# Performance work log

Measured on AMD Instinct MI355X. Metric: run time of the kernel, lower is better.

Reference implementation:

```python
import math
import jax, jax.numpy as jnp
import numpy as np

B, T, D_MODEL, HEAD_DIM = 4, 2048, 768, 64

def setup_inputs() -> dict:
    key = jax.random.key(0)
    ks = jax.random.split(key, 4)
    scale = 1.0 / math.sqrt(D_MODEL)
    return {
        "x": jax.random.normal(ks[0], (B, T, D_MODEL), dtype=jnp.float32),
        "Wq": jax.random.normal(ks[1], (D_MODEL, HEAD_DIM), dtype=jnp.float32) * scale,
        "bq": jnp.zeros((HEAD_DIM,), dtype=jnp.float32),
        "Wk": jax.random.normal(ks[2], (D_MODEL, HEAD_DIM), dtype=jnp.float32) * scale,
        "bk": jnp.zeros((HEAD_DIM,), dtype=jnp.float32),
        "Wv": jax.random.normal(ks[3], (D_MODEL, HEAD_DIM), dtype=jnp.float32) * scale,
        "bv": jnp.zeros((HEAD_DIM,), dtype=jnp.float32),
    }

def reference(x, Wq, bq, Wk, bk, Wv, bv):
    # Single causal self-attention head (dropout=0 / eval mode).
    q = x @ Wq + bq                      # [B, T, H]
    k = x @ Wk + bk                      # [B, T, H]
    v = x @ Wv + bv                      # [B, T, H]
    head_dim = q.shape[-1]
    scores = jnp.einsum("bth,bsh->bts", q, k) / math.sqrt(head_dim)  # [B, T, T]
    seq_len = x.shape[1]
    causal = jnp.tril(jnp.ones((seq_len, seq_len), dtype=bool))      # [T, T]
    scores = jnp.where(causal, scores, -jnp.inf)
    attn = jax.nn.softmax(scores, axis=-1)                           # [B, T, T]
    out = jnp.einsum("bts,bsh->bth", attn, v)                        # [B, T, H]
    return out
```

## Files before the change

### kernel.cpp

```cpp
#include <hip/hip_runtime.h>
#include <math.h>

#define BB 4
#define TT 2048
#define DM 768
#define HD 64
#define NROW (BB*TT)
#define WFRAG_HALF ((size_t)24*12*512)

typedef __attribute__((ext_vector_type(8))) short bf16x8;
typedef __attribute__((ext_vector_type(4))) float f32x4;

__device__ __forceinline__ unsigned short f2bf(float f) {
    unsigned int u = __float_as_uint(f);
    u += 0x7FFFu + ((u >> 16) & 1u);
    return (unsigned short)(u >> 16);
}
__device__ __forceinline__ float bf2f(unsigned short h) {
    return __uint_as_float(((unsigned int)h) << 16);
}

__global__ __launch_bounds__(256) void wconv_kernel(
    const float* __restrict__ Wq, const float* __restrict__ Wk,
    const float* __restrict__ Wv, unsigned short* __restrict__ wfrag)
{
    __shared__ float ws[32][69];
    const int blk = blockIdx.x;
    const int m = blk / 24, kc = blk % 24;
    const float* Wm = (m == 0) ? Wq : ((m == 1) ? Wk : Wv);
    const float sc = (m == 0) ? 0.125f : 1.0f;
    const int tid = threadIdx.x;
    {
        int r = tid >> 3, c0 = (tid & 7) * 8;
        *(float4*)&ws[r][c0]     = *(const float4*)(Wm + (size_t)(32*kc + r)*HD + c0);
        *(float4*)&ws[r][c0 + 4] = *(const float4*)(Wm + (size_t)(32*kc + r)*HD + c0 + 4);
    }
    __syncthreads();
    const int ntm = tid >> 6, lane = tid & 63;
    const int q15 = lane & 15, g = lane >> 4;
    const int col = 16*ntm + q15;
    bf16x8 hi, lo;
    #pragma unroll
    for (int j = 0; j < 8; ++j) {
        float w = ws[8*g + j][col] * sc;
        unsigned short h = f2bf(w);
        hi[j] = (short)h;
        lo[j] = (short)f2bf(w - bf2f(h));
    }
    size_t base = ((size_t)(kc*12 + m*4 + ntm))*512 + (size_t)lane*8;
    *(bf16x8*)(wfrag + base) = hi;
    *(bf16x8*)(wfrag + WFRAG_HALF + base) = lo;
}

__global__ __launch_bounds__(256, 3) void proj_mfma_kernel(
    const float* __restrict__ x, const unsigned short* __restrict__ wfrag,
    const float* __restrict__ bq, const float* __restrict__ bk,
    const float* __restrict__ bv,
    unsigned short* __restrict__ qo, unsigned short* __restrict__ ko,
    unsigned short* __restrict__ vT)
{
    __shared__ unsigned short stg[2304];
    const int tid  = threadIdx.x;
    const int wv   = tid >> 6;
    const int lane = tid & 63;
    const int q15  = lane & 15;
    const int g    = lane >> 4;
    const int bx   = blockIdx.x;
    const int nb   = bx % 3;
    const int row0 = (bx / 3) * 32;
    const int mt   = wv & 1;
    const int np   = wv >> 1;
    const int ntg0 = nb*4 + 2*np;

    const float* xp = x + (size_t)(row0 + 16*mt + q15)*DM + 8*g;

    f32x4 acc[2];
    acc[0] = (f32x4){0.f, 0.f, 0.f, 0.f};
    acc[1] = (f32x4){0.f, 0.f, 0.f, 0.f};

    for (int kcg = 0; kcg < 24; ++kcg) {
        float4 xa = *(const float4*)(xp + 32*kcg);
        float4 xb = *(const float4*)(xp + 32*kcg + 4);
        bf16x8 xfh, xfl;
        float f[8] = {xa.x, xa.y, xa.z, xa.w, xb.x, xb.y, xb.z, xb.w};
        #pragma unroll
        for (int e = 0; e < 8; ++e) {
            unsigned short h = (unsigned short)(__float_as_uint(f[e]) >> 16);
            float r = f[e] - bf2f(h);
            xfh[e] = (short)h;
            xfl[e] = (short)(unsigned short)(__float_as_uint(r) >> 16);
        }
        #pragma unroll
        for (int i = 0; i < 2; ++i) {
            const unsigned short* wp = wfrag + ((size_t)(kcg*12 + ntg0 + i))*512 + (size_t)lane*8;
            bf16x8 wh = *(const bf16x8*)wp;
            bf16x8 wl = *(const bf16x8*)(wp + WFRAG_HALF);
            acc[i] = __builtin_amdgcn_mfma_f32_16x16x32_bf16(xfh, wh, acc[i], 0, 0, 0);
            acc[i] = __builtin_amdgcn_mfma_f32_16x16x32_bf16(xfl, wh, acc[i], 0, 0, 0);
            acc[i] = __builtin_amdgcn_mfma_f32_16x16x32_bf16(xfh, wl, acc[i], 0, 0, 0);
        }
    }

    if (nb < 2) {
        const float* bp = (nb == 0) ? bq : bk;
        const float bsc = (nb == 0) ? 0.125f : 1.0f;
        #pragma unroll
        for (int i = 0; i < 2; ++i) {
            int col = 16*(2*np + i) + q15;
            float bb = bsc * bp[col];
            #pragma unroll
            for (int r = 0; r < 4; ++r)
                stg[(size_t)(16*mt + 4*g + r)*68 + col] = f2bf(acc[i][r] + bb);
        }
        __syncthreads();
        const int rr = tid >> 3;
        const int c8 = (tid & 7) * 8;
        ushort4 a  = *(const ushort4*)&stg[(size_t)rr*68 + c8];
        ushort4 b2 = *(const ushort4*)&stg[(size_t)rr*68 + c8 + 4];
        unsigned short* op = (nb == 0) ? qo : ko;
        *(ushort4*)(op + (size_t)(row0 + rr)*HD + c8)     = a;
        *(ushort4*)(op + (size_t)(row0 + rr)*HD + c8 + 4) = b2;
    } else {
        #pragma unroll
        for (int i = 0; i < 2; ++i) {
            int h = 16*(2*np + i) + q15;
            float bb = bv[h];
            ushort4 v4;
            v4.x = f2bf(acc[i][0] + bb);
            v4.y = f2bf(acc[i][1] + bb);
            v4.z = f2bf(acc[i][2] + bb);
            v4.w = f2bf(acc[i][3] + bb);
            *(ushort4*)&stg[(size_t)h*36 + 16*mt + 4*g] = v4;
        }
        __syncthreads();
        const int h  = tid >> 2;
        const int tg = (tid & 3) * 8;
        const int b  = row0 >> 11;
        const int t0 = row0 & 2047;
        ushort4 a  = *(const ushort4*)&stg[(size_t)h*36 + tg];
        ushort4 b2 = *(const ushort4*)&stg[(size_t)h*36 + tg + 4];
        *(ushort4*)(vT + ((size_t)b*HD + h)*TT + t0 + tg)     = a;
        *(ushort4*)(vT + ((size_t)b*HD + h)*TT + t0 + tg + 4) = b2;
    }
}

__global__ __launch_bounds__(256) void attn_mfma_kernel(
    const unsigned short* __restrict__ qb_, const unsigned short* __restrict__ kb_,
    const unsigned short* __restrict__ vt_, float* __restrict__ out)
{
    __shared__ unsigned short plds[4][16][40];
    __shared__ float olds[4][16][66];
    __shared__ float mlds[4][16][2];

    const int tid  = threadIdx.x;
    const int wv   = tid >> 6;
    const int lane = tid & 63;
    const int q15  = lane & 15;
    const int g    = lane >> 4;

    const int bx = blockIdx.x;
    const int b  = bx & 3;
    const int qt = (TT/16 - 1) - (bx >> 2);
    const int qbase = qt * 16;
    const int nk = qbase + 16;

    const unsigned short* qp = qb_ + (size_t)b*TT*HD;
    const unsigned short* kp = kb_ + (size_t)b*TT*HD;
    const unsigned short* vp = vt_ + (size_t)b*HD*TT;

    bf16x8 qf[2];
    #pragma unroll
    for (int c = 0; c < 2; ++c)
        qf[c] = *(const bf16x8*)(qp + (size_t)(qbase + q15)*HD + 32*c + 8*g);

    f32x4 accv[4];
    #pragma unroll
    for (int h = 0; h < 4; ++h) accv[h] = (f32x4){0.f, 0.f, 0.f, 0.f};
    float m = -INFINITY, l = 0.f;

    const int ck = ((nk + 127) >> 7) << 5;
    const int kstart = wv * ck;
    const int kend = min(kstart + ck, nk);

    for (int k0 = kstart; k0 < kend; k0 += 32) {
        bf16x8 vf[4];
        #pragma unroll
        for (int h = 0; h < 4; ++h)
            vf[h] = *(const bf16x8*)(vp + (size_t)(16*h + q15)*TT + k0 + 8*g);
        bf16x8 kf[2][2];
        #pragma unroll
        for (int t = 0; t < 2; ++t)
            #pragma unroll
            for (int c = 0; c < 2; ++c)
                kf[t][c] = *(const bf16x8*)(kp + (size_t)(k0 + 16*t + q15)*HD + 32*c + 8*g);

        f32x4 st[2];
        #pragma unroll
        for (int t = 0; t < 2; ++t) {
            f32x4 z = {0.f, 0.f, 0.f, 0.f};
            st[t] = __builtin_amdgcn_mfma_f32_16x16x32_bf16(kf[t][0], qf[0], z, 0, 0, 0);
            st[t] = __builtin_amdgcn_mfma_f32_16x16x32_bf16(kf[t][1], qf[1], st[t], 0, 0, 0);
        }
        if (k0 + 31 > qbase) {
            int qabs = qbase + q15;
            #pragma unroll
            for (int t = 0; t < 2; ++t)
                #pragma unroll
                for (int r = 0; r < 4; ++r)
                    if (k0 + 16*t + 4*g + r > qabs) st[t][r] = -INFINITY;
        }
        float pmax = st[0][0];
        #pragma unroll
        for (int t = 0; t < 2; ++t)
            #pragma unroll
            for (int r = 0; r < 4; ++r) pmax = fmaxf(pmax, st[t][r]);
        pmax = fmaxf(pmax, __shfl_xor(pmax, 16));
        pmax = fmaxf(pmax, __shfl_xor(pmax, 32));
        float mnew = fmaxf(m, pmax);
        float mc = fmaxf(mnew, -1e30f);
        float alpha = __expf(m - mc);
        float p[2][4];
        float psum = 0.f;
        #pragma unroll
        for (int t = 0; t < 2; ++t)
            #pragma unroll
            for (int r = 0; r < 4; ++r) {
                p[t][r] = __expf(st[t][r] - mc);
                psum += p[t][r];
            }
        psum += __shfl_xor(psum, 16);
        psum += __shfl_xor(psum, 32);
        l = l * alpha + psum;
        m = mnew;
        float av[4];
        #pragma unroll
        for (int r = 0; r < 4; ++r) av[r] = __shfl(alpha, 4*g + r);
        #pragma unroll
        for (int h = 0; h < 4; ++h)
            #pragma unroll
            for (int r = 0; r < 4; ++r) accv[h][r] *= av[r];
        #pragma unroll
        for (int t = 0; t < 2; ++t) {
            ushort4 pk;
            pk.x = f2bf(p[t][0]); pk.y = f2bf(p[t][1]);
            pk.z = f2bf(p[t][2]); pk.w = f2bf(p[t][3]);
            *(ushort4*)&plds[wv][q15][16*t + 4*g] = pk;
        }
        bf16x8 pa = *(const bf16x8*)&plds[wv][q15][8*g];
        #pragma unroll
        for (int h = 0; h < 4; ++h)
            accv[h] = __builtin_amdgcn_mfma_f32_16x16x32_bf16(pa, vf[h], accv[h], 0, 0, 0);
    }

    #pragma unroll
    for (int h = 0; h < 4; ++h)
        #pragma unroll
        for (int r = 0; r < 4; ++r)
            olds[wv][4*g + r][16*h + q15] = accv[h][r];
    if (g == 0) { mlds[wv][q15][0] = m; mlds[wv][q15][1] = l; }
    __syncthreads();

    {
        int qq = tid >> 4;
        int c4 = (tid & 15) << 2;
        float mw[4], lw[4];
        #pragma unroll
        for (int w = 0; w < 4; ++w) { mw[w] = mlds[w][qq][0]; lw[w] = mlds[w][qq][1]; }
        float M = fmaxf(fmaxf(mw[0], mw[1]), fmaxf(mw[2], mw[3]));
        float Mc = fmaxf(M, -1e30f);
        float ww[4], ltot = 0.f;
        #pragma unroll
        for (int w = 0; w < 4; ++w) { ww[w] = __expf(mw[w] - Mc); ltot += ww[w]*lw[w]; }
        float invl = 1.f / ltot;
        float4 o;
        #pragma unroll
        for (int e = 0; e < 4; ++e) {
            float s = 0.f;
            #pragma unroll
            for (int w = 0; w < 4; ++w) s += ww[w] * olds[w][qq][c4 + e];
            ((float*)&o)[e] = s * invl;
        }
        *(float4*)(out + ((size_t)b*TT + qbase + qq)*HD + c4) = o;
    }
}

extern "C" void kernel_launch(void* const* d_in, const int* in_sizes, int n_in,
                              void* d_out, int out_size, void* d_ws, size_t ws_size,
                              hipStream_t stream) {
    const float* x  = (const float*)d_in[0];
    const float* Wq = (const float*)d_in[1];
    const float* bq = (const float*)d_in[2];
    const float* Wk = (const float*)d_in[3];
    const float* bk = (const float*)d_in[4];
    const float* Wv = (const float*)d_in[5];
    const float* bv = (const float*)d_in[6];
    float* out = (float*)d_out;

    unsigned short* qbf   = (unsigned short*)d_ws;
    unsigned short* kbf   = qbf + (size_t)NROW*HD;
    unsigned short* vT    = kbf + (size_t)NROW*HD;
    unsigned short* wfrag = vT  + (size_t)NROW*HD;

    wconv_kernel<<<72, 256, 0, stream>>>(Wq, Wk, Wv, wfrag);
    proj_mfma_kernel<<<768, 256, 0, stream>>>(x, wfrag, bq, bk, bv, qbf, kbf, vT);
    attn_mfma_kernel<<<dim3(TT/16 * BB), 256, 0, stream>>>(qbf, kbf, vT, out);
}
```

Baseline: 61.22 us.

## Restructure projection kernel to one 16-col tile per wave with 16-row blocks

The projection kernel now uses 16-row blocks with 6 waves, where each wave owns one 16-column output tile, instead of 32-row blocks with two tiles per wave. The weight fragment layout is reordered so that each tile's K-chunks are contiguous. Epilogue staging becomes per-wave LDS with no block-wide barrier. The change aims for more parallelism and simpler stores, but each x row is now read by 12 waves across 2 blocks, raising redundant x loads and hi/lo split work compared with before.

```diff
diff --git a/kernel.cpp b/kernel.cpp
--- a/kernel.cpp
+++ b/kernel.cpp
@@ -47,100 +47,76 @@
         hi[j] = (short)h;
         lo[j] = (short)f2bf(w - bf2f(h));
     }
-    size_t base = ((size_t)(kc*12 + m*4 + ntm))*512 + (size_t)lane*8;
+    size_t base = ((size_t)((m*4 + ntm)*24 + kc))*512 + (size_t)lane*8;
     *(bf16x8*)(wfrag + base) = hi;
     *(bf16x8*)(wfrag + WFRAG_HALF + base) = lo;
 }
 
-__global__ __launch_bounds__(256, 3) void proj_mfma_kernel(
+__global__ __launch_bounds__(384) void proj_mfma_kernel(
     const float* __restrict__ x, const unsigned short* __restrict__ wfrag,
     const float* __restrict__ bq, const float* __restrict__ bk,
     const float* __restrict__ bv,
     unsigned short* __restrict__ qo, unsigned short* __restrict__ ko,
     unsigned short* __restrict__ vT)
 {
-    __shared__ unsigned short stg[2304];
+    __shared__ unsigned short tl[6][16][20];
     const int tid  = threadIdx.x;
-    const int wv   = tid >> 6;
+    const int wv   = tid / 64;
     const int lane = tid & 63;
     const int q15  = lane & 15;
     const int g    = lane >> 4;
-    const int bx   = blockIdx.x;
-    const int nb   = bx % 3;
-    const int row0 = (bx / 3) * 32;
-    const int mt   = wv & 1;
-    const int np   = wv >> 1;
-    const int ntg0 = nb*4 + 2*np;
-
-    const float* xp = x + (size_t)(row0 + 16*mt + q15)*DM + 8*g;
-
-    f32x4 acc[2];
-    acc[0] = (f32x4){0.f, 0.f, 0.f, 0.f};
-    acc[1] = (f32x4){0.f, 0.f, 0.f, 0.f};
+    const int rt   = blockIdx.x;
+    const int nt   = blockIdx.y * 6 + wv;
+    const int m    = nt >> 2, ntm = nt & 3;
+    const int row0 = rt * 16;
+
+    const float* xp = x + (size_t)(row0 + q15)*DM + 8*g;
+    const unsigned short* wbase = wfrag + (size_t)nt*24*512 + (size_t)lane*8;
+
+    f32x4 acc = (f32x4){0.f, 0.f, 0.f, 0.f};
 
     for (int kcg = 0; kcg < 24; ++kcg) {
         float4 xa = *(const float4*)(xp + 32*kcg);
         float4 xb = *(const float4*)(xp + 32*kcg + 4);
+        bf16x8 wh = *(const bf16x8*)(wbase + (size_t)kcg*512);
+        bf16x8 wl = *(const bf16x8*)(wbase + WFRAG_HALF + (size_t)kcg*512);
         bf16x8 xfh, xfl;
         float f[8] = {xa.x, xa.y, xa.z, xa.w, xb.x, xb.y, xb.z, xb.w};
         #pragma unroll
         for (int e = 0; e < 8; ++e) {
             unsigned short h = (unsigned short)(__float_as_uint(f[e]) >> 16);
-            float r = f[e] - bf2f(h);
+            float rr = f[e] - bf2f(h);
             xfh[e] = (short)h;
-            xfl[e] = (short)(unsigned short)(__float_as_uint(r) >> 16);
-        }
-        #pragma unroll
-        for (int i = 0; i < 2; ++i) {
-            const unsigned short* wp = wfrag + ((size_t)(kcg*12 + ntg0 + i))*512 + (size_t)lane*8;
-            bf16x8 wh = *(const bf16x8*)wp;
-            bf16x8 wl = *(const bf16x8*)(wp + WFRAG_HALF);
-            acc[i] = __builtin_amdgcn_mfma_f32_16x16x32_bf16(xfh, wh, acc[i], 0, 0, 0);
-            acc[i] = __builtin_amdgcn_mfma_f32_16x16x32_bf16(xfl, wh, acc[i], 0, 0, 0);
-            acc[i] = __builtin_amdgcn_mfma_f32_16x16x32_bf16(xfh, wl, acc[i], 0, 0, 0);
-        }
-    }
-
-    if (nb < 2) {
-        const float* bp = (nb == 0) ? bq : bk;
-        const float bsc = (nb == 0) ? 0.125f : 1.0f;
-        #pragma unroll
-        for (int i = 0; i < 2; ++i) {
-            int col = 16*(2*np + i) + q15;
-            float bb = bsc * bp[col];
-            #pragma unroll
-            for (int r = 0; r < 4; ++r)
-                stg[(size_t)(16*mt + 4*g + r)*68 + col] = f2bf(acc[i][r] + bb);
-        }
-        __syncthreads();
-        const int rr = tid >> 3;
-        const int c8 = (tid & 7) * 8;
-        ushort4 a  = *(const ushort4*)&stg[(size_t)rr*68 + c8];
-        ushort4 b2 = *(const ushort4*)&stg[(size_t)rr*68 + c8 + 4];
-        unsigned short* op = (nb == 0) ? qo : ko;
-        *(ushort4*)(op + (size_t)(row0 + rr)*HD + c8)     = a;
-        *(ushort4*)(op + (size_t)(row0 + rr)*HD + c8 + 4) = b2;
+            xfl[e] = (short)(unsigned short)(__float_as_uint(rr) >> 16);
+        }
+        acc = __builtin_amdgcn_mfma_f32_16x16x32_bf16(xfh, wh, acc, 0, 0, 0);
+        acc = __builtin_amdgcn_mfma_f32_16x16x32_bf16(xfl, wh, acc, 0, 0, 0);
+        acc = __builtin_amdgcn_mfma_f32_16x16x32_bf16(xfh, wl, acc, 0, 0, 0);
+    }
+
+    const int col = 16*ntm + q15;
+    const float bb = (m == 0) ? 0.125f*bq[col] : ((m == 1) ? bk[col] : bv[col]);
+    #pragma unroll
+    for (int r = 0; r < 4; ++r)
+        tl[wv][4*g + r][q15] = f2bf(acc[r] + bb);
+
+    if (m < 2) {
+        unsigned short* op = (m == 0) ? qo : ko;
+        const int row = lane >> 2;
+        const int c4  = (lane & 3) * 4;
+        ushort4 v4 = *(const ushort4*)&tl[wv][row][c4];
+        *(ushort4*)(op + (size_t)(row0 + row)*HD + 16*ntm + c4) = v4;
     } else {
-        #pragma unroll
-        for (int i = 0; i < 2; ++i) {
-            int h = 16*(2*np + i) + q15;
-            float bb = bv[h];
-            ushort4 v4;
-            v4.x = f2bf(acc[i][0] + bb);
-            v4.y = f2bf(acc[i][1] + bb);
-            v4.z = f2bf(acc[i][2] + bb);
-            v4.w = f2bf(acc[i][3] + bb);
-            *(ushort4*)&stg[(size_t)h*36 + 16*mt + 4*g] = v4;
-        }
-        __syncthreads();
-        const int h  = tid >> 2;
-        const int tg = (tid & 3) * 8;
+        const int h  = lane >> 2;
+        const int t4 = (lane & 3) * 4;
+        ushort4 v4;
+        v4.x = tl[wv][t4 + 0][h];
+        v4.y = tl[wv][t4 + 1][h];
+        v4.z = tl[wv][t4 + 2][h];
+        v4.w = tl[wv][t4 + 3][h];
         const int b  = row0 >> 11;
         const int t0 = row0 & 2047;
-        ushort4 a  = *(const ushort4*)&stg[(size_t)h*36 + tg];
-        ushort4 b2 = *(const ushort4*)&stg[(size_t)h*36 + tg + 4];
-        *(ushort4*)(vT + ((size_t)b*HD + h)*TT + t0 + tg)     = a;
-        *(ushort4*)(vT + ((size_t)b*HD + h)*TT + t0 + tg + 4) = b2;
+        *(ushort4*)(vT + ((size_t)b*HD + 16*ntm + h)*TT + t0 + t4) = v4;
     }
 }
 
@@ -302,6 +278,6 @@
     unsigned short* wfrag = vT  + (size_t)NROW*HD;
 
     wconv_kernel<<<72, 256, 0, stream>>>(Wq, Wk, Wv, wfrag);
-    proj_mfma_kernel<<<768, 256, 0, stream>>>(x, wfrag, bq, bk, bv, qbf, kbf, vT);
+    proj_mfma_kernel<<<dim3(512, 2), 384, 0, stream>>>(x, wfrag, bq, bk, bv, qbf, kbf, vT);
     attn_mfma_kernel<<<dim3(TT/16 * BB), 256, 0, stream>>>(qbf, kbf, vT, out);
 }
```

After: 75.62 us. 1.24x slower.
